# Performance work log

Measured on AMD Instinct MI355X. Metric: run time of the kernel, lower is better.

The kernel has to match this reference:

```python
import jax, jax.numpy as jnp
import numpy as np

B, D, NS, C, H = 4096, 1024, 16000, 1000, 256


def setup_inputs() -> dict:
    key = jax.random.key(0)
    ks = jax.random.split(key, 8)
    # L2-normalized image features (output of frozen CLIP encode_image + norm)
    q = jax.random.normal(ks[0], (B, D), jnp.float32)
    q = q / jnp.linalg.norm(q, axis=-1, keepdims=True)
    # zero-shot CLIP logits
    z = jax.random.normal(ks[1], (B, C), jnp.float32)
    # L2-normalized support/cache features
    keys = jax.random.normal(ks[2], (NS, D), jnp.float32)
    keys = keys / jnp.linalg.norm(keys, axis=-1, keepdims=True)
    # one-hot support labels
    labels = jax.random.randint(ks[3], (NS,), 0, C)
    values = jax.nn.one_hot(labels, C, dtype=jnp.float32)
    # gate MLP params (small init like nn.Linear default scale)
    fc1_w = jax.random.normal(ks[4], (H, D), jnp.float32) * 0.02
    fc1_b = jnp.zeros((H,), jnp.float32)
    fc2_w = jax.random.normal(ks[5], (2, H), jnp.float32) * 0.02
    fc2_b = jnp.zeros((2,), jnp.float32)
    post_scale = jnp.ones((1,), jnp.float32)
    return {"q": q, "z": z, "keys": keys, "values": values,
            "fc1_w": fc1_w, "fc1_b": fc1_b, "fc2_w": fc2_w, "fc2_b": fc2_b,
            "post_scale": post_scale}


def reference(q, z, keys, values, fc1_w, fc1_b, fc2_w, fc2_b, post_scale):
    # GateMLP: per-image alpha in (0,1), beta > 0
    x = jax.nn.relu(q @ fc1_w.T + fc1_b)            # [B, H]
    g = x @ fc2_w.T + fc2_b                          # [B, 2]
    alpha_hat = jax.nn.sigmoid(g[:, 0:1])            # [B, 1]
    beta = jax.nn.softplus(g[:, 1:2]) + 0.001        # [B, 1] (learn_beta=True)
    # cache logits: sim -> exp affinity -> label aggregation
    sim = q @ keys.T                                 # [B, Ns]
    affinity = jnp.exp(beta * sim)                   # [B, Ns]
    c = affinity @ values                            # [B, C]
    # gated convex fusion with zero-shot logits
    logits = ((1.0 - alpha_hat) * z + alpha_hat * c) * post_scale
    return (logits, alpha_hat, beta)
```

## Files before the change

### kernel.cpp

```cpp
#include <hip/hip_runtime.h>
#include <hip/hip_bf16.h>
#include <stdint.h>

#define B_  4096
#define D_  1024
#define NS_ 16000
#define C_  1000
#define H_  256
#define LBLK 4000
#define QCB  1024
#define KCB  4000
#define FCB  64
#define CONVB (QCB + KCB + FCB)
#define RSTRIDE 2048

typedef __attribute__((ext_vector_type(8))) short bf16x8;
typedef __attribute__((ext_vector_type(4))) float f32x4;
typedef __attribute__((ext_vector_type(16))) float f32x16;
typedef __attribute__((ext_vector_type(8))) int i32x8;

__device__ __forceinline__ unsigned short f2bf(float f) {
  union { float f; unsigned u; } v; v.f = f;
  unsigned u = v.u;
  u += 0x7FFF + ((u >> 16) & 1);
  return (unsigned short)(u >> 16);
}

__device__ __forceinline__ float bf2f(unsigned short h) {
  union { unsigned u; float f; } v; v.u = ((unsigned)h) << 16;
  return v.f;
}

__global__ void prep_kernel(const float4* __restrict__ q, const float4* __restrict__ keys,
                            const float4* __restrict__ fc1, const float* __restrict__ values,
                            ushort4* __restrict__ qb, int* __restrict__ q8,
                            int* __restrict__ keys8, ushort4* __restrict__ fc1b,
                            int* __restrict__ labels, int* __restrict__ hist) {
  const int bid = blockIdx.x;
  if (bid < QCB) {
    const size_t i0 = (size_t)bid * 1024 + threadIdx.x;
    #pragma unroll
    for (int k = 0; k < 4; ++k) {
      const size_t i = i0 + k * 256;
      float4 v = q[i];
      ushort4 r; r.x = f2bf(v.x); r.y = f2bf(v.y); r.z = f2bf(v.z); r.w = f2bf(v.w);
      qb[i] = r;
      int p = __builtin_amdgcn_cvt_pk_fp8_f32(v.x * 64.f, v.y * 64.f, 0, false);
      p     = __builtin_amdgcn_cvt_pk_fp8_f32(v.z * 64.f, v.w * 64.f, p, true);
      q8[i] = p;
    }
    return;
  }
  if (bid < QCB + KCB) {
    const size_t i0 = (size_t)(bid - QCB) * 1024 + threadIdx.x;
    #pragma unroll
    for (int k = 0; k < 4; ++k) {
      const size_t i = i0 + k * 256;
      float4 v = keys[i];
      int p = __builtin_amdgcn_cvt_pk_fp8_f32(v.x * 64.f, v.y * 64.f, 0, false);
      p     = __builtin_amdgcn_cvt_pk_fp8_f32(v.z * 64.f, v.w * 64.f, p, true);
      keys8[i] = p;
    }
    return;
  }
  if (bid < CONVB) {
    const size_t i0 = (size_t)(bid - QCB - KCB) * 1024 + threadIdx.x;
    #pragma unroll
    for (int k = 0; k < 4; ++k) {
      const size_t i = i0 + k * 256;
      float4 v = fc1[i];
      ushort4 r; r.x = f2bf(v.x); r.y = f2bf(v.y); r.z = f2bf(v.z); r.w = f2bf(v.w);
      fc1b[i] = r;
    }
    return;
  }
  const int s = (bid - CONVB) * 4 + (threadIdx.x >> 6);
  const int lane = threadIdx.x & 63;
  const float4* row = (const float4*)(values + (size_t)s * C_);
  int lab = -1;
  for (int j = lane; j < C_ / 4; j += 64) {
    float4 v = row[j];
    if (v.x > 0.5f) lab = j * 4 + 0;
    if (v.y > 0.5f) lab = j * 4 + 1;
    if (v.z > 0.5f) lab = j * 4 + 2;
    if (v.w > 0.5f) lab = j * 4 + 3;
    if (__ballot(lab >= 0)) break;
  }
  if (lab >= 0) { labels[s] = lab; atomicAdd(&hist[lab], 1); }
}

union MidShared {
  struct {
    short As[32 * 64];
    short Bs[256 * 64];
    float gred[4][32][2];
  } g;
  struct {
    int sscan[1024];
    int sboff[C_ + 1];
    int scnt[C_];
    unsigned short slab[NS_];
    int stile[NS_ / 128];
  } s;
};

__global__ __launch_bounds__(1024) void midpipe_kernel(
    const short* __restrict__ A, const short* __restrict__ Bm,
    const float* __restrict__ bias, const float* __restrict__ fc2_w,
    const float* __restrict__ fc2_b, float* __restrict__ ab,
    const int* __restrict__ hist, const int* __restrict__ labels,
    int* __restrict__ sortidx, int* __restrict__ runid, int* __restrict__ labstart)
{
  __shared__ MidShared u;
  const int tid = threadIdx.x;

  if (blockIdx.x < B_ / 32) {
    short* As = u.g.As;
    short* Bs = u.g.Bs;
    const bool act = tid < 256;
    const int wave = (tid >> 6) & 3, lane = tid & 63;
    const int quad = lane >> 4, l16 = lane & 15;
    const int wn = wave;
    const int rstart = blockIdx.x * 32;

    f32x4 acc[2][4];
    #pragma unroll
    for (int i = 0; i < 2; ++i)
      #pragma unroll
      for (int j = 0; j < 4; ++j) acc[i][j] = (f32x4)0.f;

    const int r_  = (lane >> 3);
    const int kc_ = ((lane & 7) ^ r_) * 8;

    for (int kt = 0; kt < D_; kt += 64) {
      __syncthreads();
      if (act) {
        {
          const int row = wave * 8 + r_;
          const short* gA = A + (size_t)(rstart + row) * D_ + kt + kc_;
          __builtin_amdgcn_global_load_lds(
              (const __attribute__((address_space(1))) void*)gA,
              (__attribute__((address_space(3))) void*)(As + wave * 512), 16, 0, 0);
        }
        #pragma unroll
        for (int i = 0; i < 8; ++i) {
          const int g = i * 4 + wave;
          const int row = g * 8 + r_;
          const short* gB = Bm + (size_t)row * D_ + kt + kc_;
          __builtin_amdgcn_global_load_lds(
              (const __attribute__((address_space(1))) void*)gB,
              (__attribute__((address_space(3))) void*)(Bs + g * 512), 16, 0, 0);
        }
      }
      __syncthreads();
      if (act) {
        #pragma unroll
        for (int ks = 0; ks < 64; ks += 32) {
          bf16x8 af[2], bfr[4];
          const int kb = (ks >> 3) + quad;
          #pragma unroll
          for (int mt = 0; mt < 2; ++mt) {
            const int row = mt * 16 + l16;
            af[mt] = *(const bf16x8*)(As + row * 64 + ((kb ^ (row & 7)) << 3));
          }
          #pragma unroll
          for (int nt = 0; nt < 4; ++nt) {
            const int row = wn * 64 + nt * 16 + l16;
            bfr[nt] = *(const bf16x8*)(Bs + row * 64 + ((kb ^ (row & 7)) << 3));
          }
          #pragma unroll
          for (int mt = 0; mt < 2; ++mt)
            #pragma unroll
            for (int nt = 0; nt < 4; ++nt)
              acc[mt][nt] = __builtin_amdgcn_mfma_f32_16x16x32_bf16(af[mt], bfr[nt], acc[mt][nt], 0, 0, 0);
        }
      }
    }

    if (act) {
      float g0p[2][4], g1p[2][4];
      #pragma unroll
      for (int mt = 0; mt < 2; ++mt)
        #pragma unroll
        for (int r = 0; r < 4; ++r) { g0p[mt][r] = 0.f; g1p[mt][r] = 0.f; }
      #pragma unroll
      for (int nt = 0; nt < 4; ++nt) {
        const int col = wn * 64 + nt * 16 + l16;
        const float bv = bias[col];
        const float w0 = fc2_w[col], w1 = fc2_w[H_ + col];
        #pragma unroll
        for (int mt = 0; mt < 2; ++mt)
          #pragma unroll
          for (int r = 0; r < 4; ++r) {
            float xv = acc[mt][nt][r] + bv;
            xv = xv > 0.f ? xv : 0.f;
            g0p[mt][r] += xv * w0;
            g1p[mt][r] += xv * w1;
          }
      }
      #pragma unroll
      for (int mt = 0; mt < 2; ++mt)
        #pragma unroll
        for (int r = 0; r < 4; ++r) {
          float a0 = g0p[mt][r], a1 = g1p[mt][r];
          #pragma unroll
          for (int off = 8; off > 0; off >>= 1) {
            a0 += __shfl_xor(a0, off);
            a1 += __shfl_xor(a1, off);
          }
          if (l16 == 0) {
            const int row = mt * 16 + quad * 4 + r;
            u.g.gred[wave][row][0] = a0;
            u.g.gred[wave][row][1] = a1;
          }
        }
    }
    __syncthreads();
    if (tid < 32) {
      float g0 = u.g.gred[0][tid][0] + u.g.gred[1][tid][0] + u.g.gred[2][tid][0] +
                 u.g.gred[3][tid][0] + fc2_b[0];
      float g1 = u.g.gred[0][tid][1] + u.g.gred[1][tid][1] + u.g.gred[2][tid][1] +
                 u.g.gred[3][tid][1] + fc2_b[1];
      ab[rstart + tid]      = 1.f / (1.f + __expf(-g0));
      ab[B_ + rstart + tid] = fmaxf(g1, 0.f) + log1pf(__expf(-fabsf(g1))) + 0.001f;
    }
    return;
  }

  const int t = tid;
  int v = (t < C_) ? hist[t] : 0;
  u.s.sscan[t] = v;
  if (t < C_) u.s.scnt[t] = 0;
  __syncthreads();
  for (int off = 1; off < 1024; off <<= 1) {
    int w = (t >= off) ? u.s.sscan[t - off] : 0;
    __syncthreads(); u.s.sscan[t] += w; __syncthreads();
  }
  if (t == 0) u.s.sboff[0] = 0;
  if (t < C_) u.s.sboff[t + 1] = u.s.sscan[t];
  __syncthreads();

  for (int s = t; s < NS_; s += 1024) {
    const int lab = labels[s];
    const int pos = u.s.sboff[lab] + atomicAdd(&u.s.scnt[lab], 1);
    sortidx[pos] = s;
    u.s.slab[pos] = (unsigned short)lab;
  }
  __syncthreads();

  const int c0 = t * 16;
  int flags[16]; int cnt = 0;
  if (c0 < NS_) {
    int prev = (c0 == 0) ? u.s.slab[0] : u.s.slab[c0 - 1];
    #pragma unroll
    for (int i = 0; i < 16; ++i) {
      const int l = u.s.slab[c0 + i];
      const int f = ((c0 + i) != 0) && (l != prev);
      flags[i] = f; cnt += f; prev = l;
    }
  }
  u.s.sscan[t] = cnt; __syncthreads();
  for (int off = 1; off < 1024; off <<= 1) {
    int w = (t >= off) ? u.s.sscan[t - off] : 0;
    __syncthreads(); u.s.sscan[t] += w; __syncthreads();
  }
  if (c0 < NS_ && (t & 7) == 0) u.s.stile[t >> 3] = (u.s.sscan[t] - cnt) + flags[0];
  __syncthreads();
  if (c0 < NS_) {
    int run = u.s.sscan[t] - cnt;
    const int base = (c0 >> 7) * 16 - u.s.stile[c0 >> 7];
    #pragma unroll
    for (int i = 0; i < 16; ++i) {
      run += flags[i];
      runid[c0 + i] = base + run;
    }
  }
  if (t == 0) runid[NS_] = (NS_ >> 7) * 16;
  __threadfence();
  __syncthreads();
  if (t <= C_) labstart[t] = runid[u.s.sboff[t]];
}

__device__ __forceinline__ i32x8 mx_frag(const char* base, int lrow, int kh, int sel) {
  const int c0 = kh * 4 + sel * 2;
  const int s = lrow & 7;
  const int4 lo = *(const int4*)(base + lrow * 128 + (((c0    ) ^ s) << 4));
  const int4 hi = *(const int4*)(base + lrow * 128 + (((c0 + 1) ^ s) << 4));
  i32x8 f;
  f[0] = lo.x; f[1] = lo.y; f[2] = lo.z; f[3] = lo.w;
  f[4] = hi.x; f[5] = hi.y; f[6] = hi.z; f[7] = hi.w;
  return f;
}

__global__ __launch_bounds__(256, 2) void mxgemm_kernel(
    const char* __restrict__ A8, const char* __restrict__ B8,
    const float* __restrict__ beta, float* __restrict__ partials,
    const int* __restrict__ sortidx, const int* __restrict__ runid)
{
  __shared__ __align__(16) char smem[32768];
  __shared__ float sbeta[128];
  __shared__ __align__(16) unsigned short Es[16 * 136];
  char* As = smem;
  char* Bs = smem + 16384;

  const int tid  = threadIdx.x;
  const int wave = tid >> 6, lane = tid & 63;
  const int sel  = lane >> 5, l32 = lane & 31;
  const int wm = wave >> 1, wn = wave & 1;
  const int rstart = blockIdx.x * 128;
  const int nstart = blockIdx.y * 128;

  for (int i = tid; i < (16 * 136) / 2; i += 256) ((int*)Es)[i] = 0;
  if (tid < 128) sbeta[tid] = beta[rstart + tid];
  __syncthreads();
  if (tid < 128) Es[(runid[nstart + tid] & 15) * 136 + tid] = 0x3F80;

  const int srow_ = (lane >> 3);
  const int gch_  = (lane & 7) ^ srow_;

  int arow[4], brow[4];
  #pragma unroll
  for (int i = 0; i < 4; ++i) {
    const int row = wave * 32 + i * 8 + srow_;
    arow[i] = rstart + row;
    brow[i] = sortidx[nstart + row];
  }

  f32x16 acc[2][2];
  #pragma unroll
  for (int i = 0; i < 2; ++i)
    #pragma unroll
    for (int j = 0; j < 2; ++j) acc[i][j] = (f32x16)0.f;

  for (int kt = 0; kt < D_; kt += 128) {
    __syncthreads();
    #pragma unroll
    for (int i = 0; i < 4; ++i) {
      const char* gA = A8 + (size_t)arow[i] * D_ + kt + (gch_ << 4);
      const char* gB = B8 + (size_t)brow[i] * D_ + kt + (gch_ << 4);
      __builtin_amdgcn_global_load_lds(
          (const __attribute__((address_space(1))) void*)gA,
          (__attribute__((address_space(3))) void*)(As + wave * 4096 + i * 1024), 16, 0, 0);
      __builtin_amdgcn_global_load_lds(
          (const __attribute__((address_space(1))) void*)gB,
          (__attribute__((address_space(3))) void*)(Bs + wave * 4096 + i * 1024), 16, 0, 0);
    }
    __syncthreads();
    #pragma unroll
    for (int kh = 0; kh < 2; ++kh) {
      i32x8 a0 = mx_frag(As, wm * 64 +  0 + l32, kh, sel);
      i32x8 a1 = mx_frag(As, wm * 64 + 32 + l32, kh, sel);
      i32x8 b0 = mx_frag(Bs, wn * 64 +  0 + l32, kh, sel);
      i32x8 b1 = mx_frag(Bs, wn * 64 + 32 + l32, kh, sel);
      acc[0][0] = __builtin_amdgcn_mfma_scale_f32_32x32x64_f8f6f4(a0, b0, acc[0][0], 0, 0, 0, 121, 0, 121);
      acc[0][1] = __builtin_amdgcn_mfma_scale_f32_32x32x64_f8f6f4(a0, b1, acc[0][1], 0, 0, 0, 121, 0, 121);
      acc[1][0] = __builtin_amdgcn_mfma_scale_f32_32x32x64_f8f6f4(a1, b0, acc[1][0], 0, 0, 0, 121, 0, 121);
      acc[1][1] = __builtin_amdgcn_mfma_scale_f32_32x32x64_f8f6f4(a1, b1, acc[1][1], 0, 0, 0, 121, 0, 121);
    }
  }

  __syncthreads();
  unsigned short* tile = (unsigned short*)smem;
  #pragma unroll
  for (int mt = 0; mt < 2; ++mt) {
    #pragma unroll
    for (int nt = 0; nt < 2; ++nt) {
      const int col = wn * 64 + nt * 32 + l32;
      const int cc = col >> 3, cl = col & 7;
      #pragma unroll
      for (int r = 0; r < 16; ++r) {
        const int row = wm * 64 + mt * 32 + (r & 3) + 8 * (r >> 2) + 4 * sel;
        const float v = __expf(sbeta[row] * acc[mt][nt][r]);
        tile[row * 128 + (((cc ^ (row & 7)) << 3) | cl)] = f2bf(v);
      }
    }
  }
  __syncthreads();

  {
    const int quad = lane >> 4, l16 = lane & 15;
    const int rowb = wave * 32;
    f32x4 racc[2];
    racc[0] = (f32x4)0.f; racc[1] = (f32x4)0.f;
    #pragma unroll
    for (int kc = 0; kc < 4; ++kc) {
      const bf16x8 bfrag = *(const bf16x8*)(Es + l16 * 136 + kc * 32 + quad * 8);
      #pragma unroll
      for (int rg = 0; rg < 2; ++rg) {
        const int row = rowb + rg * 16 + l16;
        const int kch = kc * 4 + quad;
        const bf16x8 afrag = *(const bf16x8*)(tile + row * 128 + ((kch ^ (row & 7)) << 3));
        racc[rg] = __builtin_amdgcn_mfma_f32_16x16x32_bf16(afrag, bfrag, racc[rg], 0, 0, 0);
      }
    }
    const int tb = (nstart >> 7) * 16;
    #pragma unroll
    for (int rg = 0; rg < 2; ++rg) {
      #pragma unroll
      for (int r = 0; r < 4; ++r) {
        const int row = rowb + rg * 16 + quad * 4 + r;
        partials[(size_t)(rstart + row) * RSTRIDE + tb + l16] = racc[rg][r];
      }
    }
  }
}

__global__ __launch_bounds__(256) void reduce_kernel(
    const float* __restrict__ partials, const int* __restrict__ labstart,
    const float* __restrict__ z, const float* __restrict__ ps, float* __restrict__ out) {
  __shared__ __align__(16) float sp[RSTRIDE];
  __shared__ int sls[C_ + 1];
  const int b = blockIdx.x;
  const int t = threadIdx.x;
  for (int i = t; i <= C_; i += 256) sls[i] = labstart[i];
  const float4* p4 = (const float4*)(partials + (size_t)b * RSTRIDE);
  float4* s4 = (float4*)sp;
  for (int i = t; i < RSTRIDE / 4; i += 256) s4[i] = p4[i];
  __syncthreads();
  const float a  = out[(size_t)B_ * C_ + b];
  const float sc = ps[0];
  for (int lab = t; lab < C_; lab += 256) {
    float c = 0.f;
    for (int j = sls[lab]; j < sls[lab + 1]; ++j) c += sp[j];
    const size_t oi = (size_t)b * C_ + lab;
    out[oi] = ((1.f - a) * z[oi] + a * c) * sc;
  }
}

extern "C" void kernel_launch(void* const* d_in, const int* in_sizes, int n_in,
                              void* d_out, int out_size, void* d_ws, size_t ws_size,
                              hipStream_t stream) {
  const float* q          = (const float*)d_in[0];
  const float* z          = (const float*)d_in[1];
  const float* keys       = (const float*)d_in[2];
  const float* values     = (const float*)d_in[3];
  const float* fc1_w      = (const float*)d_in[4];
  const float* fc1_b      = (const float*)d_in[5];
  const float* fc2_w      = (const float*)d_in[6];
  const float* fc2_b      = (const float*)d_in[7];
  const float* post_scale = (const float*)d_in[8];
  float* out = (float*)d_out;

  char* ws = (char*)d_ws;
  short* qb        = (short*)(ws);
  char*  q8        = (char*) (ws +  8388608);
  char*  keys8     = (char*) (ws + 12582912);
  short* fc1b      = (short*)(ws + 28966912);
  int*   labels    = (int*)  (ws + 29491200);
  int*   hist      = (int*)  (ws + 33749504);
  int*   sortidx   = (int*)  (ws + 33761792);
  int*   runid     = (int*)  (ws + 33889792);
  int*   labstart  = (int*)  (ws + 33953808);
  float* partials  = (float*)(ws + 33959936);

  float* alpha = out + (size_t)B_ * C_;
  float* beta  = alpha + B_;

  hipMemsetAsync(hist, 0, 4096, stream);

  prep_kernel<<<CONVB + LBLK, 256, 0, stream>>>(
      (const float4*)q, (const float4*)keys, (const float4*)fc1_w, values,
      (ushort4*)qb, (int*)q8, (int*)keys8, (ushort4*)fc1b, labels, hist);

  midpipe_kernel<<<B_ / 32 + 1, 1024, 0, stream>>>(
      qb, fc1b, fc1_b, fc2_w, fc2_b, alpha, hist, labels, sortidx, runid, labstart);

  mxgemm_kernel<<<dim3(B_ / 128, NS_ / 128), 256, 0, stream>>>(
      q8, keys8, beta, partials, sortidx, runid);

  reduce_kernel<<<B_, 256, 0, stream>>>(partials, labstart, z, post_scale, out);
}
```

Baseline: 320.7 us.

## Load A fragments directly from global and compute label histogram in shared memory

```diff
diff --git a/kernel.cpp b/kernel.cpp
--- a/kernel.cpp
+++ b/kernel.cpp
@@ -35,7 +35,7 @@
                             const float4* __restrict__ fc1, const float* __restrict__ values,
                             ushort4* __restrict__ qb, int* __restrict__ q8,
                             int* __restrict__ keys8, ushort4* __restrict__ fc1b,
-                            int* __restrict__ labels, int* __restrict__ hist) {
+                            int* __restrict__ labels) {
   const int bid = blockIdx.x;
   if (bid < QCB) {
     const size_t i0 = (size_t)bid * 1024 + threadIdx.x;
@@ -86,7 +86,7 @@
     if (v.w > 0.5f) lab = j * 4 + 3;
     if (__ballot(lab >= 0)) break;
   }
-  if (lab >= 0) { labels[s] = lab; atomicAdd(&hist[lab], 1); }
+  if (lab >= 0) labels[s] = lab;
 }
 
 union MidShared {
@@ -108,7 +108,7 @@
     const short* __restrict__ A, const short* __restrict__ Bm,
     const float* __restrict__ bias, const float* __restrict__ fc2_w,
     const float* __restrict__ fc2_b, float* __restrict__ ab,
-    const int* __restrict__ hist, const int* __restrict__ labels,
+    const int* __restrict__ labels,
     int* __restrict__ sortidx, int* __restrict__ runid, int* __restrict__ labstart)
 {
   __shared__ MidShared u;
@@ -228,10 +228,15 @@
   }
 
   const int t = tid;
-  int v = (t < C_) ? hist[t] : 0;
+  if (t < C_) u.s.scnt[t] = 0;
+  __syncthreads();
+  for (int s = t; s < NS_; s += 1024)
+    atomicAdd(&u.s.scnt[labels[s]], 1);
+  __syncthreads();
+  int v = (t < C_) ? u.s.scnt[t] : 0;
   u.s.sscan[t] = v;
+  __syncthreads();
   if (t < C_) u.s.scnt[t] = 0;
-  __syncthreads();
   for (int off = 1; off < 1024; off <<= 1) {
     int w = (t >= off) ? u.s.sscan[t - off] : 0;
     __syncthreads(); u.s.sscan[t] += w; __syncthreads();
@@ -292,6 +297,15 @@
   return f;
 }
 
+__device__ __forceinline__ i32x8 mx_frag_g(const char* p) {
+  const int4 lo = *(const int4*)(p);
+  const int4 hi = *(const int4*)(p + 16);
+  i32x8 f;
+  f[0] = lo.x; f[1] = lo.y; f[2] = lo.z; f[3] = lo.w;
+  f[4] = hi.x; f[5] = hi.y; f[6] = hi.z; f[7] = hi.w;
+  return f;
+}
+
 __global__ __launch_bounds__(256, 2) void mxgemm_kernel(
     const char* __restrict__ A8, const char* __restrict__ B8,
     const float* __restrict__ beta, float* __restrict__ partials,
@@ -300,7 +314,6 @@
   __shared__ __align__(16) char smem[32768];
   __shared__ float sbeta[128];
   __shared__ __align__(16) unsigned short Es[16 * 136];
-  char* As = smem;
   char* Bs = smem + 16384;
 
   const int tid  = threadIdx.x;
@@ -318,13 +331,13 @@
   const int srow_ = (lane >> 3);
   const int gch_  = (lane & 7) ^ srow_;
 
-  int arow[4], brow[4];
+  int brow[4];
   #pragma unroll
-  for (int i = 0; i < 4; ++i) {
-    const int row = wave * 32 + i * 8 + srow_;
-    arow[i] = rstart + row;
-    brow[i] = sortidx[nstart + row];
-  }
+  for (int i = 0; i < 4; ++i)
+    brow[i] = sortidx[nstart + wave * 32 + i * 8 + srow_];
+
+  const char* pa0 = A8 + (size_t)(rstart + wm * 64 + l32) * D_;
+  const char* pa1 = pa0 + (size_t)32 * D_;
 
   f32x16 acc[2][2];
   #pragma unroll
@@ -336,11 +349,7 @@
     __syncthreads();
     #pragma unroll
     for (int i = 0; i < 4; ++i) {
-      const char* gA = A8 + (size_t)arow[i] * D_ + kt + (gch_ << 4);
       const char* gB = B8 + (size_t)brow[i] * D_ + kt + (gch_ << 4);
-      __builtin_amdgcn_global_load_lds(
-          (const __attribute__((address_space(1))) void*)gA,
-          (__attribute__((address_space(3))) void*)(As + wave * 4096 + i * 1024), 16, 0, 0);
       __builtin_amdgcn_global_load_lds(
           (const __attribute__((address_space(1))) void*)gB,
           (__attribute__((address_space(3))) void*)(Bs + wave * 4096 + i * 1024), 16, 0, 0);
@@ -348,8 +357,9 @@
     __syncthreads();
     #pragma unroll
     for (int kh = 0; kh < 2; ++kh) {
-      i32x8 a0 = mx_frag(As, wm * 64 +  0 + l32, kh, sel);
-      i32x8 a1 = mx_frag(As, wm * 64 + 32 + l32, kh, sel);
+      const int ko = kt + kh * 64 + sel * 32;
+      i32x8 a0 = mx_frag_g(pa0 + ko);
+      i32x8 a1 = mx_frag_g(pa1 + ko);
       i32x8 b0 = mx_frag(Bs, wn * 64 +  0 + l32, kh, sel);
       i32x8 b1 = mx_frag(Bs, wn * 64 + 32 + l32, kh, sel);
       acc[0][0] = __builtin_amdgcn_mfma_scale_f32_32x32x64_f8f6f4(a0, b0, acc[0][0], 0, 0, 0, 121, 0, 121);
@@ -447,7 +457,6 @@
   char*  keys8     = (char*) (ws + 12582912);
   short* fc1b      = (short*)(ws + 28966912);
   int*   labels    = (int*)  (ws + 29491200);
-  int*   hist      = (int*)  (ws + 33749504);
   int*   sortidx   = (int*)  (ws + 33761792);
   int*   runid     = (int*)  (ws + 33889792);
   int*   labstart  = (int*)  (ws + 33953808);
@@ -456,14 +465,12 @@
   float* alpha = out + (size_t)B_ * C_;
   float* beta  = alpha + B_;
 
-  hipMemsetAsync(hist, 0, 4096, stream);
-
   prep_kernel<<<CONVB + LBLK, 256, 0, stream>>>(
       (const float4*)q, (const float4*)keys, (const float4*)fc1_w, values,
-      (ushort4*)qb, (int*)q8, (int*)keys8, (ushort4*)fc1b, labels, hist);
+      (ushort4*)qb, (int*)q8, (int*)keys8, (ushort4*)fc1b, labels);
 
   midpipe_kernel<<<B_ / 32 + 1, 1024, 0, stream>>>(
-      qb, fc1b, fc1_b, fc2_w, fc2_b, alpha, hist, labels, sortidx, runid, labstart);
+      qb, fc1b, fc1_b, fc2_w, fc2_b, alpha, labels, sortidx, runid, labstart);
 
   mxgemm_kernel<<<dim3(B_ / 128, NS_ / 128), 256, 0, stream>>>(
       q8, keys8, beta, partials, sortidx, runid);
```

After: 364.1 us. 1.14x slower.
